# Performance work log

Hardware: AMD Instinct MI355X
Metric: run time of the kernel (lower is better)

## Reference

```python
import jax, jax.numpy as jnp
import numpy as np

N_PEDS = 4096
GRID_N = 16          # grid is GRID_N x GRID_N cells
CELL_SIDE = 0.6      # meters per cell
POOL_DIM = 2         # DIRECTIONAL pooling: relative (vx, vy)
OUT_DIM = 256
H_DIM = 128
AREA = 20.0          # scene is AREA x AREA meters


def setup_inputs() -> dict:
    key = jax.random.key(0)
    k1, k2, k3, k4, k5 = jax.random.split(key, 5)
    positions = jax.random.uniform(k1, (N_PEDS, 2), dtype=jnp.float32) * AREA
    # past position = current minus a small per-step displacement (~pedestrian velocity)
    past_positions = positions - jax.random.normal(k2, (N_PEDS, 2), dtype=jnp.float32) * 0.4
    h = jax.random.normal(k3, (N_PEDS, H_DIM), dtype=jnp.float32)
    in_dim = GRID_N * GRID_N * POOL_DIM
    scale = 1.0 / np.sqrt(in_dim)
    W_emb = jax.random.uniform(k4, (OUT_DIM, in_dim), dtype=jnp.float32, minval=-scale, maxval=scale)
    b_emb = jax.random.uniform(k5, (OUT_DIM,), dtype=jnp.float32, minval=-scale, maxval=scale)
    return {"h": h, "positions": positions, "past_positions": past_positions,
            "W_emb": W_emb, "b_emb": b_emb}


def _directional_grid(positions, past_positions):
    """DIRECTIONAL grid pooling: bin neighbours' relative velocities into an
    n x n grid (cell_side meters per cell) centred on each pedestrian, averaging
    contributions per cell (norm_cell=True). Returns [N, n*n, 2]."""
    n = GRID_N
    num = positions.shape[0]
    vel = positions - past_positions                         # [N, 2]
    rel_pos = positions[None, :, :] - positions[:, None, :]  # [N, N, 2] pos_j - pos_i
    rel_vel = vel[None, :, :] - vel[:, None, :]              # [N, N, 2] vel_j - vel_i
    # cell indices: floor(rel/cell + n/2)
    oij = jnp.floor(rel_pos / CELL_SIDE + n / 2).astype(jnp.int32)  # [N, N, 2]
    in_range = jnp.all((oij >= 0) & (oij < n), axis=-1)             # [N, N]
    valid = in_range & ~jnp.eye(num, dtype=bool)                    # exclude self
    cell_idx = jnp.where(valid, oij[..., 0] * n + oij[..., 1], 0)   # [N, N]
    vals = jnp.where(valid[..., None], rel_vel, 0.0)                # [N, N, 2]
    rows = jnp.arange(num)[:, None]                                 # [N, 1]
    grid = jnp.zeros((num, n * n, POOL_DIM), dtype=positions.dtype)
    grid = grid.at[rows, cell_idx].add(vals)                        # scatter-add values
    cnt = jnp.zeros((num, n * n), dtype=positions.dtype)
    cnt = cnt.at[rows, cell_idx].add(valid.astype(positions.dtype)) # occupancy counts
    grid = grid / jnp.maximum(cnt, 1.0)[..., None]                  # norm_cell: mean per cell
    return grid


def reference(h, positions, past_positions, W_emb, b_emb):
    grid = _directional_grid(positions, past_positions)      # [N, n*n, 2]
    flat = grid.reshape(grid.shape[0], -1)                   # [N, n*n*2]
    return jax.nn.relu(flat @ W_emb.T + b_emb)               # [N, out_dim]
```

## Files before the change

kernel.cpp:

```cpp
#include <hip/hip_runtime.h>

typedef __attribute__((ext_vector_type(4))) float f32x4;
typedef __attribute__((ext_vector_type(8))) short bf16x8;

#define NP 4096
#define IB 2

__device__ __forceinline__ unsigned short f2bf(float f) {
  unsigned int u = __float_as_uint(f);
  u = u + 0x7FFFu + ((u >> 16) & 1u);
  return (unsigned short)(u >> 16);
}

__global__ __launch_bounds__(256, 8) void pool_kernel(
    const float2* __restrict__ pos, const float2* __restrict__ past,
    const float* __restrict__ W, unsigned short* __restrict__ Wb,
    unsigned short* __restrict__ gridws) {
  __shared__ unsigned long long acc[IB][256];
  const int tid = threadIdx.x;
  const int tx = tid & (IB - 1);
  const int ty = tid >> 1;
  const int ibase = blockIdx.x * IB;
  const int i = ibase + tx;

  if (tid < 8) {
    int idx = blockIdx.x * 64 + tid * 8;
    float4 w0 = *(const float4*)&W[idx];
    float4 w1 = *(const float4*)&W[idx + 4];
    bf16x8 bv;
    bv[0] = (short)f2bf(w0.x); bv[1] = (short)f2bf(w0.y);
    bv[2] = (short)f2bf(w0.z); bv[3] = (short)f2bf(w0.w);
    bv[4] = (short)f2bf(w1.x); bv[5] = (short)f2bf(w1.y);
    bv[6] = (short)f2bf(w1.z); bv[7] = (short)f2bf(w1.w);
    *(bf16x8*)&Wb[idx] = bv;
  }

  for (int idx = tid; idx < IB * 256 * 2; idx += 256)
    ((unsigned int*)acc)[idx] = 0u;
  __syncthreads();

  const float2 pi = pos[i];
  const float2 qi = past[i];
  const float vix = pi.x - qi.x;
  const float viy = pi.y - qi.y;
  unsigned long long* accp = acc[tx];
  const float inv06 = 1.0f / 0.6f;

  auto process = [&](float2 pj, float2 qj) {
    float rx = pj.x - pi.x;
    float ry = pj.y - pi.y;
    float ax = __builtin_fmaf(rx, inv06, 8.0f);
    float ay = __builtin_fmaf(ry, inv06, 8.0f);
    bool unc = (fabsf(ax - rintf(ax)) < 1e-4f) |
               (fabsf(ay - rintf(ay)) < 1e-4f);
    float fx, fy;
    if (__any(unc)) {
      fx = floorf(rx / 0.6f + 8.0f);
      fy = floorf(ry / 0.6f + 8.0f);
    } else {
      fx = floorf(ax);
      fy = floorf(ay);
    }
    int ix = (int)fx;
    int iy = (int)fy;
    if (((unsigned)ix < 16u) & ((unsigned)iy < 16u)) {
      float rvx = (pj.x - qj.x) - vix;
      float rvy = (pj.y - qj.y) - viy;
      unsigned int qx = (unsigned int)((int)rintf(rvx * 2048.0f) + 16384);
      unsigned int qy = (unsigned int)((int)rintf(rvy * 2048.0f) + 16384);
      unsigned long long p = ((unsigned long long)qx << 38) |
                             ((unsigned long long)qy << 12) | 1ull;
      atomicAdd(&accp[(ix << 4) + iy], p);
    }
  };

  for (int jo = 0; jo < NP; jo += 512) {
    int j0 = jo + ty;
    float2 p0 = pos[j0];        float2 q0 = past[j0];
    float2 p1 = pos[j0 + 128];  float2 q1 = past[j0 + 128];
    float2 p2 = pos[j0 + 256];  float2 q2 = past[j0 + 256];
    float2 p3 = pos[j0 + 384];  float2 q3 = past[j0 + 384];
    process(p0, q0);
    process(p1, q1);
    process(p2, q2);
    process(p3, q3);
  }
  __syncthreads();

  const int cell = tid;
  const float selfc = (cell == 136) ? 1.0f : 0.0f;
#pragma unroll
  for (int il = 0; il < IB; ++il) {
    unsigned long long raw = acc[il][cell];
    unsigned int cnt = (unsigned int)(raw & 0xFFFull);
    int sxq = (int)((unsigned int)(raw >> 38)) - (int)(cnt << 14);
    int syq = (int)((unsigned int)((raw >> 12) & 0x3FFFFFFull)) - (int)(cnt << 14);
    float cn = (float)cnt - selfc;
    float d = fmaxf(cn, 1.0f);
    float sx = (float)sxq * (1.0f / 2048.0f);
    float sy = (float)syq * (1.0f / 2048.0f);
    unsigned int packed =
        ((unsigned int)f2bf(sy / d) << 16) | (unsigned int)f2bf(sx / d);
    *(unsigned int*)&gridws[(size_t)(ibase + il) * 512 + cell * 2] = packed;
  }
}

__global__ __launch_bounds__(512) void gemm_kernel(
    const unsigned short* __restrict__ A, const unsigned short* __restrict__ Wb,
    const float* __restrict__ bias, float* __restrict__ out) {
  __shared__ float red[8][32][65];
  const int tid = threadIdx.x;
  const int lane = tid & 63;
  const int w = tid >> 6;
  const int mbase = blockIdx.x * 32;
  const int nbase = blockIdx.y * 64;
  const int lrow = lane & 15;
  const int lk8 = (lane >> 4) * 8;
  const int k0 = w * 64;

  bf16x8 a[2][2], b[2][4];
#pragma unroll
  for (int ks = 0; ks < 2; ++ks) {
    const int kk = k0 + ks * 32 + lk8;
#pragma unroll
    for (int mf = 0; mf < 2; ++mf)
      a[ks][mf] = *(const bf16x8*)&A[(size_t)(mbase + mf * 16 + lrow) * 512 + kk];
#pragma unroll
    for (int nf = 0; nf < 4; ++nf)
      b[ks][nf] = *(const bf16x8*)&Wb[(size_t)(nbase + nf * 16 + lrow) * 512 + kk];
  }

  f32x4 acc[2][4] = {};
#pragma unroll
  for (int ks = 0; ks < 2; ++ks)
#pragma unroll
    for (int mf = 0; mf < 2; ++mf)
#pragma unroll
      for (int nf = 0; nf < 4; ++nf)
        acc[mf][nf] = __builtin_amdgcn_mfma_f32_16x16x32_bf16(
            a[ks][mf], b[ks][nf], acc[mf][nf], 0, 0, 0);

  const int rq = (lane >> 4) * 4;
#pragma unroll
  for (int mf = 0; mf < 2; ++mf)
#pragma unroll
    for (int nf = 0; nf < 4; ++nf)
#pragma unroll
      for (int q = 0; q < 4; ++q)
        red[w][mf * 16 + rq + q][nf * 16 + lrow] = acc[mf][nf][q];
  __syncthreads();

  const int m = tid >> 4;
  const int nq = (tid & 15) * 4;
  float s0 = 0.f, s1 = 0.f, s2 = 0.f, s3 = 0.f;
#pragma unroll
  for (int w2 = 0; w2 < 8; ++w2) {
    s0 += red[w2][m][nq + 0];
    s1 += red[w2][m][nq + 1];
    s2 += red[w2][m][nq + 2];
    s3 += red[w2][m][nq + 3];
  }
  const float4 bv = *(const float4*)&bias[nbase + nq];
  float4 o;
  o.x = fmaxf(s0 + bv.x, 0.0f);
  o.y = fmaxf(s1 + bv.y, 0.0f);
  o.z = fmaxf(s2 + bv.z, 0.0f);
  o.w = fmaxf(s3 + bv.w, 0.0f);
  *(float4*)&out[(size_t)(mbase + m) * 256 + nbase + nq] = o;
}

extern "C" void kernel_launch(void* const* d_in, const int* in_sizes, int n_in,
                              void* d_out, int out_size, void* d_ws, size_t ws_size,
                              hipStream_t stream) {
  const float2* pos = (const float2*)d_in[1];
  const float2* past = (const float2*)d_in[2];
  const float* W = (const float*)d_in[3];
  const float* bias = (const float*)d_in[4];
  float* out = (float*)d_out;

  unsigned short* gridws = (unsigned short*)d_ws;
  unsigned short* Wb = (unsigned short*)((char*)d_ws + 4 * 1024 * 1024);

  pool_kernel<<<NP / IB, 256, 0, stream>>>(pos, past, W, Wb, gridws);
  dim3 g(NP / 32, 256 / 64);
  gemm_kernel<<<g, 512, 0, stream>>>(gridws, Wb, bias, out);
  gemm_kernel<<<g, 512, 0, stream>>>(gridws, Wb, bias, out);
}
```

Baseline: 41.80 us.

## Pool four pedestrians per block, shrink GEMM tiles, drop duplicate GEMM launch

The pooling kernel now handles four centre pedestrians per block, and each thread loads one neighbour and tests it against all four. This amortises the neighbour loads and reduces the grid to 1024 blocks. The GEMM kernel is retiled to 16 rows by 64 columns with 4 waves, each covering 128 K, and the reduction uses vectorised LDS accesses. The redundant second GEMM launch is removed. More pedestrians per block means fewer blocks, which may lower occupancy or load balance, and LDS atomic contention on each centre's cells may rise.

After: 35.99 us. 13.9% less time.

```diff
diff --git a/kernel.cpp b/kernel.cpp
--- a/kernel.cpp
+++ b/kernel.cpp
@@ -4,7 +4,6 @@
 typedef __attribute__((ext_vector_type(8))) short bf16x8;
 
 #define NP 4096
-#define IB 2
 
 __device__ __forceinline__ unsigned short f2bf(float f) {
   unsigned int u = __float_as_uint(f);
@@ -16,15 +15,12 @@
     const float2* __restrict__ pos, const float2* __restrict__ past,
     const float* __restrict__ W, unsigned short* __restrict__ Wb,
     unsigned short* __restrict__ gridws) {
-  __shared__ unsigned long long acc[IB][256];
+  __shared__ unsigned long long acc[4][256];
   const int tid = threadIdx.x;
-  const int tx = tid & (IB - 1);
-  const int ty = tid >> 1;
-  const int ibase = blockIdx.x * IB;
-  const int i = ibase + tx;
+  const int ibase = blockIdx.x * 4;
 
-  if (tid < 8) {
-    int idx = blockIdx.x * 64 + tid * 8;
+  if (tid < 16) {
+    int idx = blockIdx.x * 128 + tid * 8;
     float4 w0 = *(const float4*)&W[idx];
     float4 w1 = *(const float4*)&W[idx + 4];
     bf16x8 bv;
@@ -35,63 +31,62 @@
     *(bf16x8*)&Wb[idx] = bv;
   }
 
-  for (int idx = tid; idx < IB * 256 * 2; idx += 256)
-    ((unsigned int*)acc)[idx] = 0u;
+  for (int idx = tid; idx < 1024; idx += 256)
+    ((unsigned long long*)acc)[idx] = 0ull;
   __syncthreads();
 
-  const float2 pi = pos[i];
-  const float2 qi = past[i];
-  const float vix = pi.x - qi.x;
-  const float viy = pi.y - qi.y;
-  unsigned long long* accp = acc[tx];
+  float2 pip[4];
+  float vix[4], viy[4];
+#pragma unroll
+  for (int t = 0; t < 4; ++t) {
+    float2 p = pos[ibase + t];
+    float2 q = past[ibase + t];
+    pip[t] = p;
+    vix[t] = p.x - q.x;
+    viy[t] = p.y - q.y;
+  }
   const float inv06 = 1.0f / 0.6f;
 
-  auto process = [&](float2 pj, float2 qj) {
-    float rx = pj.x - pi.x;
-    float ry = pj.y - pi.y;
-    float ax = __builtin_fmaf(rx, inv06, 8.0f);
-    float ay = __builtin_fmaf(ry, inv06, 8.0f);
-    bool unc = (fabsf(ax - rintf(ax)) < 1e-4f) |
-               (fabsf(ay - rintf(ay)) < 1e-4f);
-    float fx, fy;
-    if (__any(unc)) {
-      fx = floorf(rx / 0.6f + 8.0f);
-      fy = floorf(ry / 0.6f + 8.0f);
-    } else {
-      fx = floorf(ax);
-      fy = floorf(ay);
+  for (int jo = 0; jo < NP; jo += 256) {
+    const int j = jo + tid;
+    const float2 pj = pos[j];
+    const float2 qj = past[j];
+    const float vjx = pj.x - qj.x;
+    const float vjy = pj.y - qj.y;
+#pragma unroll
+    for (int t = 0; t < 4; ++t) {
+      float rx = pj.x - pip[t].x;
+      float ry = pj.y - pip[t].y;
+      float ax = __builtin_fmaf(rx, inv06, 8.0f);
+      float ay = __builtin_fmaf(ry, inv06, 8.0f);
+      bool unc = (fabsf(ax - rintf(ax)) < 1e-4f) |
+                 (fabsf(ay - rintf(ay)) < 1e-4f);
+      float fx, fy;
+      if (__any(unc)) {
+        fx = floorf(rx / 0.6f + 8.0f);
+        fy = floorf(ry / 0.6f + 8.0f);
+      } else {
+        fx = floorf(ax);
+        fy = floorf(ay);
+      }
+      int ix = (int)fx;
+      int iy = (int)fy;
+      if (((unsigned)ix < 16u) & ((unsigned)iy < 16u)) {
+        unsigned int qx = (unsigned int)((int)rintf((vjx - vix[t]) * 2048.0f) + 16384);
+        unsigned int qy = (unsigned int)((int)rintf((vjy - viy[t]) * 2048.0f) + 16384);
+        unsigned long long p = ((unsigned long long)qx << 38) |
+                               ((unsigned long long)qy << 12) | 1ull;
+        atomicAdd(&acc[t][(ix << 4) + iy], p);
+      }
     }
-    int ix = (int)fx;
-    int iy = (int)fy;
-    if (((unsigned)ix < 16u) & ((unsigned)iy < 16u)) {
-      float rvx = (pj.x - qj.x) - vix;
-      float rvy = (pj.y - qj.y) - viy;
-      unsigned int qx = (unsigned int)((int)rintf(rvx * 2048.0f) + 16384);
-      unsigned int qy = (unsigned int)((int)rintf(rvy * 2048.0f) + 16384);
-      unsigned long long p = ((unsigned long long)qx << 38) |
-                             ((unsigned long long)qy << 12) | 1ull;
-      atomicAdd(&accp[(ix << 4) + iy], p);
-    }
-  };
-
-  for (int jo = 0; jo < NP; jo += 512) {
-    int j0 = jo + ty;
-    float2 p0 = pos[j0];        float2 q0 = past[j0];
-    float2 p1 = pos[j0 + 128];  float2 q1 = past[j0 + 128];
-    float2 p2 = pos[j0 + 256];  float2 q2 = past[j0 + 256];
-    float2 p3 = pos[j0 + 384];  float2 q3 = past[j0 + 384];
-    process(p0, q0);
-    process(p1, q1);
-    process(p2, q2);
-    process(p3, q3);
   }
   __syncthreads();
 
   const int cell = tid;
   const float selfc = (cell == 136) ? 1.0f : 0.0f;
 #pragma unroll
-  for (int il = 0; il < IB; ++il) {
-    unsigned long long raw = acc[il][cell];
+  for (int t = 0; t < 4; ++t) {
+    unsigned long long raw = acc[t][cell];
     unsigned int cnt = (unsigned int)(raw & 0xFFFull);
     int sxq = (int)((unsigned int)(raw >> 38)) - (int)(cnt << 14);
     int syq = (int)((unsigned int)((raw >> 12) & 0x3FFFFFFull)) - (int)(cnt << 14);
@@ -101,72 +96,60 @@
     float sy = (float)syq * (1.0f / 2048.0f);
     unsigned int packed =
         ((unsigned int)f2bf(sy / d) << 16) | (unsigned int)f2bf(sx / d);
-    *(unsigned int*)&gridws[(size_t)(ibase + il) * 512 + cell * 2] = packed;
+    *(unsigned int*)&gridws[(size_t)(ibase + t) * 512 + cell * 2] = packed;
   }
 }
 
-__global__ __launch_bounds__(512) void gemm_kernel(
+__global__ __launch_bounds__(256) void gemm_kernel(
     const unsigned short* __restrict__ A, const unsigned short* __restrict__ Wb,
     const float* __restrict__ bias, float* __restrict__ out) {
-  __shared__ float red[8][32][65];
+  __shared__ float red[4][64][20];
   const int tid = threadIdx.x;
   const int lane = tid & 63;
   const int w = tid >> 6;
-  const int mbase = blockIdx.x * 32;
+  const int mbase = blockIdx.x * 16;
   const int nbase = blockIdx.y * 64;
   const int lrow = lane & 15;
   const int lk8 = (lane >> 4) * 8;
-  const int k0 = w * 64;
 
-  bf16x8 a[2][2], b[2][4];
+  f32x4 acc[4] = {};
 #pragma unroll
-  for (int ks = 0; ks < 2; ++ks) {
-    const int kk = k0 + ks * 32 + lk8;
+  for (int ksp = 0; ksp < 4; ksp += 2) {
+    bf16x8 a[2], b[2][4];
 #pragma unroll
-    for (int mf = 0; mf < 2; ++mf)
-      a[ks][mf] = *(const bf16x8*)&A[(size_t)(mbase + mf * 16 + lrow) * 512 + kk];
-#pragma unroll
-    for (int nf = 0; nf < 4; ++nf)
-      b[ks][nf] = *(const bf16x8*)&Wb[(size_t)(nbase + nf * 16 + lrow) * 512 + kk];
-  }
-
-  f32x4 acc[2][4] = {};
-#pragma unroll
-  for (int ks = 0; ks < 2; ++ks)
-#pragma unroll
-    for (int mf = 0; mf < 2; ++mf)
+    for (int u = 0; u < 2; ++u) {
+      const int k0 = w * 128 + (ksp + u) * 32 + lk8;
+      a[u] = *(const bf16x8*)&A[(size_t)(mbase + lrow) * 512 + k0];
 #pragma unroll
       for (int nf = 0; nf < 4; ++nf)
-        acc[mf][nf] = __builtin_amdgcn_mfma_f32_16x16x32_bf16(
-            a[ks][mf], b[ks][nf], acc[mf][nf], 0, 0, 0);
+        b[u][nf] = *(const bf16x8*)&Wb[(size_t)(nbase + nf * 16 + lrow) * 512 + k0];
+    }
+#pragma unroll
+    for (int u = 0; u < 2; ++u)
+#pragma unroll
+      for (int nf = 0; nf < 4; ++nf)
+        acc[nf] = __builtin_amdgcn_mfma_f32_16x16x32_bf16(
+            a[u], b[u][nf], acc[nf], 0, 0, 0);
+  }
 
   const int rq = (lane >> 4) * 4;
 #pragma unroll
-  for (int mf = 0; mf < 2; ++mf)
-#pragma unroll
-    for (int nf = 0; nf < 4; ++nf)
-#pragma unroll
-      for (int q = 0; q < 4; ++q)
-        red[w][mf * 16 + rq + q][nf * 16 + lrow] = acc[mf][nf][q];
+  for (int nf = 0; nf < 4; ++nf)
+    *(f32x4*)&red[w][nf * 16 + lrow][rq] = acc[nf];
   __syncthreads();
 
-  const int m = tid >> 4;
-  const int nq = (tid & 15) * 4;
-  float s0 = 0.f, s1 = 0.f, s2 = 0.f, s3 = 0.f;
+  const int col = tid & 63;
+  const int mq = (tid >> 6) * 4;
+  f32x4 s = {};
 #pragma unroll
-  for (int w2 = 0; w2 < 8; ++w2) {
-    s0 += red[w2][m][nq + 0];
-    s1 += red[w2][m][nq + 1];
-    s2 += red[w2][m][nq + 2];
-    s3 += red[w2][m][nq + 3];
+  for (int w2 = 0; w2 < 4; ++w2) {
+    f32x4 r = *(const f32x4*)&red[w2][col][mq];
+    s += r;
   }
-  const float4 bv = *(const float4*)&bias[nbase + nq];
-  float4 o;
-  o.x = fmaxf(s0 + bv.x, 0.0f);
-  o.y = fmaxf(s1 + bv.y, 0.0f);
-  o.z = fmaxf(s2 + bv.z, 0.0f);
-  o.w = fmaxf(s3 + bv.w, 0.0f);
-  *(float4*)&out[(size_t)(mbase + m) * 256 + nbase + nq] = o;
+  const float bv = bias[nbase + col];
+#pragma unroll
+  for (int q = 0; q < 4; ++q)
+    out[(size_t)(mbase + mq + q) * 256 + nbase + col] = fmaxf(s[q] + bv, 0.0f);
 }
 
 extern "C" void kernel_launch(void* const* d_in, const int* in_sizes, int n_in,
@@ -181,8 +164,7 @@
   unsigned short* gridws = (unsigned short*)d_ws;
   unsigned short* Wb = (unsigned short*)((char*)d_ws + 4 * 1024 * 1024);
 
-  pool_kernel<<<NP / IB, 256, 0, stream>>>(pos, past, W, Wb, gridws);
-  dim3 g(NP / 32, 256 / 64);
-  gemm_kernel<<<g, 512, 0, stream>>>(gridws, Wb, bias, out);
-  gemm_kernel<<<g, 512, 0, stream>>>(gridws, Wb, bias, out);
+  pool_kernel<<<NP / 4, 256, 0, stream>>>(pos, past, W, Wb, gridws);
+  dim3 g(NP / 16, 256 / 64);
+  gemm_kernel<<<g, 256, 0, stream>>>(gridws, Wb, bias, out);
 }
```
